# Kernel tuning notes

Measured on AMD Instinct MI355X. Metric: run time of the kernel, lower is better.

The kernel has to match this reference:

```python
import jax, jax.numpy as jnp
import numpy as np

EPS = 1e-06


def setup_inputs() -> dict:
    key = jax.random.key(0)
    ks = jax.random.split(key, 8)
    B, T, D = 4, 1024, 1024  # module requires T == D (diagonal einsum)
    s = 1.0 / np.sqrt(D)
    return {
        "x_seq": jax.random.normal(ks[0], (B, T, D), dtype=jnp.float32),
        "gamma": jnp.asarray(0.9, dtype=jnp.float32),
        "Wq": jax.random.normal(ks[1], (D, D), dtype=jnp.float32) * s,
        "bq": jax.random.normal(ks[2], (D,), dtype=jnp.float32) * 0.01,
        "Wk": jax.random.normal(ks[3], (D, D), dtype=jnp.float32) * s,
        "bk": jax.random.normal(ks[4], (D,), dtype=jnp.float32) * 0.01,
        "Wv": jax.random.normal(ks[5], (D, D), dtype=jnp.float32) * s,
        "bv": jax.random.normal(ks[6], (D,), dtype=jnp.float32) * 0.01,
    }


def reference(x_seq, gamma, Wq, bq, Wk, bk, Wv, bv):
    # Faithful math of SUPRAParallelFixedGamma.forward. Notes on fidelity:
    # - torch einsum 'ij,bjdj->bidj' takes the DIAGONAL of kv over (time, last
    #   v-dim), i.e. kv[b,j,d,j] = k[b,j,d] * v[b,j,j]; requires T == D.
    # - gamma_exponents = arange(T)[None,:] - arange(T)[:,None] -> E[i,j] = max(j-i, 0)
    #   (the clamp leaves PAST entries at gamma**0 == 1 and decays FUTURE ones).
    # - S = cumsum over dim 1 (the 'i'/time-output axis) then contracted with q;
    #   this factors exactly as C = cumsum(G, axis=0) applied as a (T,T) weight,
    #   avoiding the original's O(B*T*D*T) intermediate while computing the same math.
    B, T, D = x_seq.shape
    q = jax.nn.relu(x_seq @ Wq.T + bq)          # phi(W_q x)
    k = jax.nn.relu(x_seq @ Wk.T + bk)          # phi(W_k x)
    v = x_seq @ Wv.T + bv
    t = jnp.arange(T)
    E = jnp.maximum(t[None, :] - t[:, None], 0).astype(x_seq.dtype)  # (T,T)
    G = gamma ** E                               # gamma_powers[i,j] = gamma**max(j-i,0)
    C = jnp.cumsum(G, axis=0)                    # C[t,j] = sum_{t'<=t} G[t',j]
    vd = jnp.diagonal(v, axis1=1, axis2=2)       # (B,T): v[b,j,j]  (T==D)
    kv_diag = k * vd[:, :, None]                 # (B,T,D): kv[b,j,d,j]
    # num[b,t,j] = sum_d q[b,t,d] * C[t,j] * kv_diag[b,j,d]
    num = C[None, :, :] * jnp.einsum('btd,bjd->btj', q, kv_diag)
    # Z[b,t,d] = cumsum_t of (G @ k) = sum_j C[t,j] k[b,j,d]
    Z = jnp.einsum('tj,bjd->btd', C, k)
    denom = jnp.sum(q * Z, axis=-1, keepdims=True) + EPS
    return num / denom
```

## Files before the change

kernel.cpp:

```cpp
#include <hip/hip_runtime.h>

typedef __attribute__((ext_vector_type(8))) short bf16x8;
typedef __attribute__((ext_vector_type(4))) float f32x4;


__device__ __forceinline__ unsigned short f2bf(float f) {
    unsigned int u = __builtin_bit_cast(unsigned int, f);
    u += 0x7fffu + ((u >> 16) & 1u);
    return (unsigned short)(u >> 16);
}

__device__ __forceinline__ float bf2f(unsigned short s) {
    return __builtin_bit_cast(float, (unsigned int)s << 16);
}

__device__ __forceinline__ void g2lds16(const unsigned short* g, unsigned short* l) {
    __builtin_amdgcn_global_load_lds(
        (const __attribute__((address_space(1))) unsigned int*)g,
        (__attribute__((address_space(3))) unsigned int*)l, 16, 0, 0);
}


__global__ __launch_bounds__(256)
void prep_kernel(const float* __restrict__ x, const float* __restrict__ wq,
                 const float* __restrict__ wk, const float* __restrict__ Wv,
                 const float* __restrict__ bv, unsigned short* __restrict__ xb,
                 unsigned short* __restrict__ wqk, float* __restrict__ vd,
                 int M, int n4w) {
    const int tid = threadIdx.x;
    if ((int)blockIdx.x < M) {
        const int row = blockIdx.x;
        const int j = row & 1023;
        const int e4 = row * 256 + tid;
        float4 v = reinterpret_cast<const float4*>(x)[e4];
        union { unsigned short s[4]; uint2 u; } o;
        o.s[0] = f2bf(v.x); o.s[1] = f2bf(v.y); o.s[2] = f2bf(v.z); o.s[3] = f2bf(v.w);
        reinterpret_cast<uint2*>(xb)[e4] = o.u;

        float4 w = reinterpret_cast<const float4*>(Wv + (size_t)j * 1024)[tid];
        float s = v.x * w.x + v.y * w.y + v.z * w.z + v.w * w.w;
        #pragma unroll
        for (int off = 32; off; off >>= 1) s += __shfl_down(s, off, 64);
        __shared__ float red[4];
        if ((tid & 63) == 0) red[tid >> 6] = s;
        __syncthreads();
        if (tid == 0) vd[row] = red[0] + red[1] + red[2] + red[3] + bv[j];
    } else {
        int i = (blockIdx.x - M) * 256 + tid;
        const float* src; int idx;
        if (i < n4w) { src = wq; idx = i; }
        else         { src = wk; idx = i; }
        float4 v = reinterpret_cast<const float4*>(src)[idx - (i < n4w ? 0 : n4w)];
        union { unsigned short s[4]; uint2 u; } o;
        o.s[0] = f2bf(v.x); o.s[1] = f2bf(v.y); o.s[2] = f2bf(v.z); o.s[3] = f2bf(v.w);
        reinterpret_cast<uint2*>(wqk)[i] = o.u;
    }
}


__global__ __launch_bounds__(256, 2)
void gemm_qk_kernel(const unsigned short* __restrict__ A, const unsigned short* __restrict__ Bm,
                    unsigned short* __restrict__ qb, unsigned short* __restrict__ kb,
                    const float* __restrict__ bq, const float* __restrict__ bk, int K) {
    __shared__ unsigned short lA[2][128 * 32];
    __shared__ unsigned short lB[2][128 * 32];

    const int tid = threadIdx.x;
    const int lane = tid & 63;
    const int wid = tid >> 6;
    const int wr = wid >> 1;
    const int wc = wid & 1;
    const int tileM = blockIdx.y * 128, tileN = blockIdx.x * 128;

    const int srow = tid >> 2;
    const int scolL = (tid & 3) * 8;
    const int scolG = ((tid & 3) ^ (srow & 3)) * 8;
    const int frow = lane & 15;
    const int fq = lane >> 4;
    const int gR = (fq ^ (frow & 3)) * 8;

    f32x4 acc[4][4];
    #pragma unroll
    for (int m = 0; m < 4; ++m)
        #pragma unroll
        for (int n = 0; n < 4; ++n)
            acc[m][n] = (f32x4){0.f, 0.f, 0.f, 0.f};

    auto stage = [&](int buf, int k0) {
        g2lds16(A + (size_t)(tileM + srow) * K + (k0 + scolG),      &lA[buf][srow * 32 + scolL]);
        g2lds16(A + (size_t)(tileM + 64 + srow) * K + (k0 + scolG), &lA[buf][(64 + srow) * 32 + scolL]);
        g2lds16(Bm + (size_t)(tileN + srow) * K + (k0 + scolG),     &lB[buf][srow * 32 + scolL]);
        g2lds16(Bm + (size_t)(tileN + 64 + srow) * K + (k0 + scolG),&lB[buf][(64 + srow) * 32 + scolL]);
    };

    stage(0, 0);
    __syncthreads();
    int cur = 0;
    for (int k0 = 0; k0 < K; k0 += 32) {
        if (k0 + 32 < K) stage(cur ^ 1, k0 + 32);

        bf16x8 af[4], bfr[4];
        #pragma unroll
        for (int m = 0; m < 4; ++m)
            af[m] = *reinterpret_cast<const bf16x8*>(
                &lA[cur][(wr * 64 + m * 16 + frow) * 32 + gR]);
        #pragma unroll
        for (int n = 0; n < 4; ++n)
            bfr[n] = *reinterpret_cast<const bf16x8*>(
                &lB[cur][(wc * 64 + n * 16 + frow) * 32 + gR]);

        #pragma unroll
        for (int m = 0; m < 4; ++m)
            #pragma unroll
            for (int n = 0; n < 4; ++n)
                acc[m][n] = __builtin_amdgcn_mfma_f32_16x16x32_bf16(af[m], bfr[n], acc[m][n], 0, 0, 0);

        __syncthreads();
        cur ^= 1;
    }

    const int orow = (lane >> 4) * 4;
    const int ocol = lane & 15;
    const bool isQ = tileN < 1024;
    unsigned short* Cq = isQ ? qb : kb;
    const float* bias = isQ ? bq : bk;
    const int cb = tileN - (isQ ? 0 : 1024);

    #pragma unroll
    for (int n = 0; n < 4; ++n) {
        int col = cb + wc * 64 + n * 16 + ocol;
        float bia = bias[col];
        #pragma unroll
        for (int m = 0; m < 4; ++m) {
            #pragma unroll
            for (int i = 0; i < 4; ++i) {
                int row = tileM + wr * 64 + m * 16 + orow + i;
                float v = acc[m][n][i] + bia;
                Cq[(size_t)row * 1024 + col] = f2bf(v > 0.f ? v : 0.f);
            }
        }
    }
}


__global__ __launch_bounds__(256, 3)
void gemm_attn_kernel(const unsigned short* __restrict__ A, const unsigned short* __restrict__ Bm,
                      unsigned short* __restrict__ nmb, const float* __restrict__ vd,
                      float* __restrict__ dpart, const float* __restrict__ gammap,
                      int K, int Mtot) {
    __shared__ unsigned short lA[2][64 * 32];
    __shared__ unsigned short lB[2][128 * 32];

    const int tid = threadIdx.x;
    const int lane = tid & 63;
    const int wid = tid >> 6;
    const int wr = wid >> 1, wc = wid & 1;
    const int tileM = blockIdx.y * 64, tileN = blockIdx.x * 128;

    const unsigned short* Ab = A + (size_t)blockIdx.z * 1024 * 1024;
    const unsigned short* Bb = Bm + (size_t)blockIdx.z * 1024 * 1024;

    const int r0 = tid >> 2;
    const int r1 = (tid + 256) >> 2;
    const int cc = (tid & 3) * 8;
    const int frow = lane & 15;
    const int fk = (lane >> 4) * 8;

    f32x4 acc[2][4];
    #pragma unroll
    for (int m = 0; m < 2; ++m)
        #pragma unroll
        for (int n = 0; n < 4; ++n)
            acc[m][n] = (f32x4){0.f, 0.f, 0.f, 0.f};

    auto stage = [&](int buf, int k0) {
        g2lds16(Ab + (size_t)(tileM + r0) * K + (k0 + cc), &lA[buf][tid * 8]);
        g2lds16(Bb + (size_t)(tileN + r0) * K + (k0 + cc), &lB[buf][tid * 8]);
        g2lds16(Bb + (size_t)(tileN + r1) * K + (k0 + cc), &lB[buf][2048 + tid * 8]);
    };

    stage(0, 0);
    __syncthreads();
    int cur = 0;
    for (int k0 = 0; k0 < K; k0 += 32) {
        if (k0 + 32 < K) stage(cur ^ 1, k0 + 32);

        bf16x8 af[2], bfr[4];
        #pragma unroll
        for (int m = 0; m < 2; ++m)
            af[m] = *reinterpret_cast<const bf16x8*>(&lA[cur][(wr * 32 + m * 16 + frow) * 32 + fk]);
        #pragma unroll
        for (int n = 0; n < 4; ++n)
            bfr[n] = *reinterpret_cast<const bf16x8*>(&lB[cur][(wc * 64 + n * 16 + frow) * 32 + fk]);

        #pragma unroll
        for (int m = 0; m < 2; ++m)
            #pragma unroll
            for (int n = 0; n < 4; ++n)
                acc[m][n] = __builtin_amdgcn_mfma_f32_16x16x32_bf16(af[m], bfr[n], acc[m][n], 0, 0, 0);

        __syncthreads();
        cur ^= 1;
    }

    const int orow = (lane >> 4) * 4;
    const int ocol = lane & 15;

    unsigned short* ob = nmb + (size_t)blockIdx.z * 1024 * 1024;
    const float* vdb = vd + blockIdx.z * 1024;
    const float g = gammap[0];
    const float l2g = log2f(g);
    const float inv1mg = 1.f / (1.f - g);
    const float c1 = g * inv1mg;

    int jcol[4]; float gj[4], vdv[4];
    #pragma unroll
    for (int n = 0; n < 4; ++n) {
        jcol[n] = tileN + wc * 64 + n * 16 + ocol;
        gj[n] = exp2f((float)jcol[n] * l2g);
        vdv[n] = vdb[jcol[n]];
    }

    #pragma unroll
    for (int m = 0; m < 2; ++m) {
        #pragma unroll
        for (int i = 0; i < 4; ++i) {
            int t = tileM + wr * 32 + m * 16 + orow + i;
            float gt = exp2f((float)t * l2g);
            float ctf = (1.f - g * gt) * inv1mg;
            float s = 0.f;
            #pragma unroll
            for (int n = 0; n < 4; ++n) {
                int j = jcol[n];
                float Cfut = exp2f((float)(j - t) * l2g) * ctf;
                float Cpast = (float)(t - j + 1) + c1 * (1.f - gj[n]);
                float Cw = (j <= t) ? Cpast : Cfut;
                float v = acc[m][n][i];
                s += Cw * v;
                ob[(size_t)t * 1024 + j] = f2bf(Cw * vdv[n] * v);
            }
            s += __shfl_xor(s, 1, 64);
            s += __shfl_xor(s, 2, 64);
            s += __shfl_xor(s, 4, 64);
            s += __shfl_xor(s, 8, 64);
            if ((lane & 15) == 0)
                dpart[(size_t)(blockIdx.x * 2 + wc) * Mtot + blockIdx.z * 1024 + t] = s;
        }
    }
}


__global__ __launch_bounds__(256)
void scale_kernel(const unsigned short* __restrict__ nmb, float* __restrict__ out,
                  const float* __restrict__ dpart, int Mtot) {
    int r = blockIdx.x;
    float s = 1e-6f;
    #pragma unroll
    for (int p = 0; p < 16; ++p) s += dpart[(size_t)p * Mtot + r];
    float inv = 1.f / s;
    const uint2* src = reinterpret_cast<const uint2*>(nmb + (size_t)r * 1024);
    float4* dst = reinterpret_cast<float4*>(out + (size_t)r * 1024);
    uint2 u = src[threadIdx.x];
    float4 v = { bf2f((unsigned short)(u.x & 0xffff)) * inv,
                 bf2f((unsigned short)(u.x >> 16))    * inv,
                 bf2f((unsigned short)(u.y & 0xffff)) * inv,
                 bf2f((unsigned short)(u.y >> 16))    * inv };
    dst[threadIdx.x] = v;
}


extern "C" void kernel_launch(void* const* d_in, const int* in_sizes, int n_in,
                              void* d_out, int out_size, void* d_ws, size_t ws_size,
                              hipStream_t stream) {
    const float* x     = (const float*)d_in[0];
    const float* gamma = (const float*)d_in[1];
    const float* Wq    = (const float*)d_in[2];
    const float* bq    = (const float*)d_in[3];
    const float* Wk    = (const float*)d_in[4];
    const float* bk    = (const float*)d_in[5];
    const float* Wv    = (const float*)d_in[6];
    const float* bv    = (const float*)d_in[7];
    float* out = (float*)d_out;

    const int D = 1024, T = 1024;
    const int B = in_sizes[0] / (T * D);
    const int M = B * T;

    char* ws = (char*)d_ws;
    size_t off = 0;
    unsigned short* xb  = (unsigned short*)(ws + off); off += (size_t)M * D * 2;
    unsigned short* wqk = (unsigned short*)(ws + off); off += (size_t)2 * D * D * 2;
    unsigned short* qb  = (unsigned short*)(ws + off); off += (size_t)M * D * 2;
    unsigned short* kb  = (unsigned short*)(ws + off); off += (size_t)M * D * 2;
    float* vd    = (float*)(ws + off); off += (size_t)M * 4;
    float* dpart = (float*)(ws + off); off += (size_t)16 * M * 4;
    unsigned short* nmb = xb;

    const int n4w = D * D / 4;

    prep_kernel<<<dim3(M + 2 * n4w / 256), 256, 0, stream>>>(
        x, Wq, Wk, Wv, bv, xb, wqk, vd, M, n4w);

    gemm_qk_kernel<<<dim3(2048 / 128, M / 128), 256, 0, stream>>>(
        xb, wqk, qb, kb, bq, bk, D);

    gemm_attn_kernel<<<dim3(T / 128, T / 64, B), 256, 0, stream>>>(
        qb, kb, nmb, vd, dpart, gamma, D, M);

    scale_kernel<<<dim3(M), 256, 0, stream>>>(nmb, out, dpart, M);
}
```

Baseline: 71.89 us.

## Fuse denominator normalization into attention GEMM via per-stripe inter-block barrier

Removes the separate scale kernel and the bf16 numerator buffer. Each attention GEMM block keeps its scaled numerator in registers, then waits on a per-row-stripe atomic counter until all 8 column blocks have written their partial denominators. It then sums the partials and writes fp32 output directly. This saves a full bf16 write and read of the numerator plus a kernel launch, but adds a spin-wait whose progress depends on all 8 blocks of a stripe being co-resident or scheduled, a deadlock risk if occupancy is insufficient.

```diff
diff --git a/kernel.cpp b/kernel.cpp
--- a/kernel.cpp
+++ b/kernel.cpp
@@ -8,10 +8,6 @@
     unsigned int u = __builtin_bit_cast(unsigned int, f);
     u += 0x7fffu + ((u >> 16) & 1u);
     return (unsigned short)(u >> 16);
-}
-
-__device__ __forceinline__ float bf2f(unsigned short s) {
-    return __builtin_bit_cast(float, (unsigned int)s << 16);
 }
 
 __device__ __forceinline__ void g2lds16(const unsigned short* g, unsigned short* l) {
@@ -26,8 +22,9 @@
                  const float* __restrict__ wk, const float* __restrict__ Wv,
                  const float* __restrict__ bv, unsigned short* __restrict__ xb,
                  unsigned short* __restrict__ wqk, float* __restrict__ vd,
-                 int M, int n4w) {
+                 int* __restrict__ ready, int M, int n4w) {
     const int tid = threadIdx.x;
+    if (blockIdx.x == 0 && tid < 64) ready[tid] = 0;
     if ((int)blockIdx.x < M) {
         const int row = blockIdx.x;
         const int j = row & 1023;
@@ -47,10 +44,10 @@
         if (tid == 0) vd[row] = red[0] + red[1] + red[2] + red[3] + bv[j];
     } else {
         int i = (blockIdx.x - M) * 256 + tid;
-        const float* src; int idx;
-        if (i < n4w) { src = wq; idx = i; }
-        else         { src = wk; idx = i; }
-        float4 v = reinterpret_cast<const float4*>(src)[idx - (i < n4w ? 0 : n4w)];
+        const float* src;
+        if (i < n4w) { src = wq; }
+        else         { src = wk; }
+        float4 v = reinterpret_cast<const float4*>(src)[i - (i < n4w ? 0 : n4w)];
         union { unsigned short s[4]; uint2 u; } o;
         o.s[0] = f2bf(v.x); o.s[1] = f2bf(v.y); o.s[2] = f2bf(v.z); o.s[3] = f2bf(v.w);
         reinterpret_cast<uint2*>(wqk)[i] = o.u;
@@ -145,9 +142,9 @@
 
 __global__ __launch_bounds__(256, 3)
 void gemm_attn_kernel(const unsigned short* __restrict__ A, const unsigned short* __restrict__ Bm,
-                      unsigned short* __restrict__ nmb, const float* __restrict__ vd,
-                      float* __restrict__ dpart, const float* __restrict__ gammap,
-                      int K, int Mtot) {
+                      float* __restrict__ out, const float* __restrict__ vd,
+                      float* __restrict__ dpart, int* __restrict__ ready,
+                      const float* __restrict__ gammap, int K, int Mtot) {
     __shared__ unsigned short lA[2][64 * 32];
     __shared__ unsigned short lB[2][128 * 32];
 
@@ -206,7 +203,7 @@
     const int orow = (lane >> 4) * 4;
     const int ocol = lane & 15;
 
-    unsigned short* ob = nmb + (size_t)blockIdx.z * 1024 * 1024;
+    float* ob = out + (size_t)blockIdx.z * 1024 * 1024;
     const float* vdb = vd + blockIdx.z * 1024;
     const float g = gammap[0];
     const float l2g = log2f(g);
@@ -237,7 +234,7 @@
                 float Cw = (j <= t) ? Cpast : Cfut;
                 float v = acc[m][n][i];
                 s += Cw * v;
-                ob[(size_t)t * 1024 + j] = f2bf(Cw * vdv[n] * v);
+                acc[m][n][i] = Cw * vdv[n] * v;
             }
             s += __shfl_xor(s, 1, 64);
             s += __shfl_xor(s, 2, 64);
@@ -247,25 +244,42 @@
                 dpart[(size_t)(blockIdx.x * 2 + wc) * Mtot + blockIdx.z * 1024 + t] = s;
         }
     }
-}
-
-
-__global__ __launch_bounds__(256)
-void scale_kernel(const unsigned short* __restrict__ nmb, float* __restrict__ out,
-                  const float* __restrict__ dpart, int Mtot) {
-    int r = blockIdx.x;
-    float s = 1e-6f;
-    #pragma unroll
-    for (int p = 0; p < 16; ++p) s += dpart[(size_t)p * Mtot + r];
-    float inv = 1.f / s;
-    const uint2* src = reinterpret_cast<const uint2*>(nmb + (size_t)r * 1024);
-    float4* dst = reinterpret_cast<float4*>(out + (size_t)r * 1024);
-    uint2 u = src[threadIdx.x];
-    float4 v = { bf2f((unsigned short)(u.x & 0xffff)) * inv,
-                 bf2f((unsigned short)(u.x >> 16))    * inv,
-                 bf2f((unsigned short)(u.y & 0xffff)) * inv,
-                 bf2f((unsigned short)(u.y >> 16))    * inv };
-    dst[threadIdx.x] = v;
+
+    const int stripe = blockIdx.z * 16 + blockIdx.y;
+    __threadfence();
+    __syncthreads();
+    if (tid == 0) {
+        atomicAdd(&ready[stripe], 1);
+        while (__hip_atomic_load(&ready[stripe], __ATOMIC_ACQUIRE,
+                                 __HIP_MEMORY_SCOPE_AGENT) < 8)
+            __builtin_amdgcn_s_sleep(2);
+        __threadfence();
+    }
+    __syncthreads();
+
+    __shared__ float inv_s[64];
+    if (tid < 64) {
+        float dsum = 1e-6f;
+        #pragma unroll
+        for (int p = 0; p < 16; ++p)
+            dsum += __hip_atomic_load(&dpart[(size_t)p * Mtot + blockIdx.z * 1024 + tileM + tid],
+                                      __ATOMIC_RELAXED, __HIP_MEMORY_SCOPE_AGENT);
+        inv_s[tid] = 1.f / dsum;
+    }
+    __syncthreads();
+
+    #pragma unroll
+    for (int m = 0; m < 2; ++m) {
+        #pragma unroll
+        for (int i = 0; i < 4; ++i) {
+            int tl = wr * 32 + m * 16 + orow + i;
+            float inv = inv_s[tl];
+            size_t rowoff = (size_t)(tileM + tl) * 1024;
+            #pragma unroll
+            for (int n = 0; n < 4; ++n)
+                ob[rowoff + jcol[n]] = acc[m][n][i] * inv;
+        }
+    }
 }
 
 
@@ -294,18 +308,16 @@
     unsigned short* kb  = (unsigned short*)(ws + off); off += (size_t)M * D * 2;
     float* vd    = (float*)(ws + off); off += (size_t)M * 4;
     float* dpart = (float*)(ws + off); off += (size_t)16 * M * 4;
-    unsigned short* nmb = xb;
+    int* ready   = (int*)(ws + off);   off += 64 * 4;
 
     const int n4w = D * D / 4;
 
     prep_kernel<<<dim3(M + 2 * n4w / 256), 256, 0, stream>>>(
-        x, Wq, Wk, Wv, bv, xb, wqk, vd, M, n4w);
+        x, Wq, Wk, Wv, bv, xb, wqk, vd, ready, M, n4w);
 
     gemm_qk_kernel<<<dim3(2048 / 128, M / 128), 256, 0, stream>>>(
         xb, wqk, qb, kb, bq, bk, D);
 
     gemm_attn_kernel<<<dim3(T / 128, T / 64, B), 256, 0, stream>>>(
-        qb, kb, nmb, vd, dpart, gamma, D, M);
-
-    scale_kernel<<<dim3(M), 256, 0, stream>>>(nmb, out, dpart, M);
-}
+        qb, kb, out, vd, dpart, ready, gamma, D, M);
+}
```

After: 120.8 us. 1.68x slower.
